# Optimization experiments

Hardware: AMD Instinct MI355X
Metric: run time of the kernel (lower is better)

The kernel has to match this reference:

```python
import jax, jax.numpy as jnp
import numpy as np

BANDS = np.array([0, 1, 2, 3, 4])
LOG_STDEVS = (0.0, 1.0)
CLAHE_MIN_STDEV = 1.0
K = 9      # CLAHE kernel size (hardcoded in module)
PAD = 4    # CLAHE reflect padding (hardcoded in module)


def _box_mean(x):
    # x: [B, C, H, W]; mean over KxK sliding window with reflect padding,
    # identical math to torch Unfold + mean over the K*K window axis.
    p = jnp.pad(x, ((0, 0), (0, 0), (PAD, PAD), (PAD, PAD)), mode='reflect')
    s = jax.lax.reduce_window(p, jnp.float32(0.0), jax.lax.add,
                              (1, 1, K, K), (1, 1, 1, 1), 'VALID')
    return s / (K * K)


def _clahe(img5d, min_stdev):
    # img5d: [B, C, 1, H, W]
    x = img5d[:, :, 0]
    res = x - _box_mean(x)
    stdev = jnp.sqrt(_box_mean(res * res))
    return (res / jnp.maximum(stdev, min_stdev))[:, :, None]


def setup_inputs() -> dict:
    key = jax.random.key(0)
    k1, k2 = jax.random.split(key, 2)
    B, C, H, W = 8, 5, 512, 512
    T = 3
    images = jax.random.normal(k1, (B, C, H, W), jnp.float32) * 10.0 + 100.0
    # background must be positive (asserted > 1e-6 in the module)
    background = jax.random.uniform(k2, (B, C, H, W), jnp.float32) * 50.0 + 50.0
    # learnable asinh params, initialized exactly as in __init__
    asinh_thresholds = jnp.tile(
        jnp.array([0.0, 1.0, 10.0], jnp.float32).reshape(1, 1, T, 1, 1),
        (1, C, 1, 1, 1))
    asinh_scales = jnp.full((1, C, T, 1, 1), np.log(0.1), jnp.float32)
    return {'images': images, 'background': background,
            'asinh_thresholds': asinh_thresholds, 'asinh_scales': asinh_scales}


def reference(images, background, asinh_thresholds, asinh_scales):
    raw = images[:, BANDS][:, :, None]        # [B, C, 1, H, W]
    bg = background[:, BANDS][:, :, None]     # [B, C, 1, H, W]
    inputs = [raw]                            # include_original=True; asinh on -> no raw background channel
    for t in LOG_STDEVS:
        off = (raw - bg) / jnp.sqrt(bg) - t
        inputs.append(jnp.log(jnp.maximum(off + 1.0, 1.0)))
    inputs.append(_clahe(raw, CLAHE_MIN_STDEV))
    inputs.append(jnp.arcsinh((raw - asinh_thresholds) * jnp.exp(asinh_scales)))
    return jnp.concatenate(inputs, axis=2)    # [B, C, 7, H, W]
```

## Files before the change

### kernel.cpp

```cpp
#include <hip/hip_runtime.h>
#include <math.h>

#define IMG_H 512
#define IMG_W 512
#define TS 32
#define NC 5
#define NB 8

__device__ __forceinline__ int reflect_idx(int i, int n) {
    if (i < 0) i = -i;
    if (i >= n) i = 2 * n - 2 - i;
    return i;
}

__device__ __forceinline__ float fast_log(float x) {
    return __builtin_amdgcn_logf(x) * 0.6931471805599453f;
}

__device__ __forceinline__ float fast_asinh(float v) {
    float a = fabsf(v);
    float r = fast_log(a + __builtin_amdgcn_sqrtf(fmaf(a, a, 1.0f)));
    return copysignf(r, v);
}

__global__ __launch_bounds__(256)
void imnorm_kernel(const float* __restrict__ img, const float* __restrict__ bgr,
                   const float* __restrict__ thr, const float* __restrict__ scl,
                   float* __restrict__ out)
{
    const int plane = blockIdx.z;
    const int c = plane % NC;
    const int h0 = blockIdx.y * TS;
    const int w0 = blockIdx.x * TS;
    const bool edge_w = (w0 == 0) || (w0 + TS == IMG_W);
    const bool edge_h = (h0 == 0) || (h0 + TS == IMG_H);

    const float* x  = img + (size_t)plane * IMG_H * IMG_W;
    const float* bg = bgr + (size_t)plane * IMG_H * IMG_W;
    float* op = out + (size_t)plane * 7 * IMG_H * IMG_W;

    const int t = threadIdx.y * 32 + threadIdx.x;

    __shared__ float xs[48][49];
    __shared__ float rs[40][41];
    __shared__ float pool[48 * 41];
    float (*h1)[41] = reinterpret_cast<float (*)[41]>(pool);
    float (*h2)[33] = reinterpret_cast<float (*)[33]>(pool);

    float s_thr[3], s_exp[3];
    #pragma unroll
    for (int j = 0; j < 3; ++j) {
        s_thr[j] = thr[c * 3 + j];
        s_exp[j] = __builtin_amdgcn_exp2f(scl[c * 3 + j] * 1.4426950408889634f);
    }

    if (!edge_w && !edge_h) {
        const float* src = x + (size_t)(h0 - 8) * IMG_W + (w0 - 8);
        #pragma unroll
        for (int k = 0; k < 9; ++k) {
            int i = t + k * 256;
            int r = i / 48, cc = i - r * 48;
            xs[r][cc] = src[r * IMG_W + cc];
        }
    } else {
        #pragma unroll
        for (int k = 0; k < 9; ++k) {
            int i = t + k * 256;
            int r = i / 48, cc = i - r * 48;
            int gr = reflect_idx(h0 - 8 + r, IMG_H);
            int gc = reflect_idx(w0 - 8 + cc, IMG_W);
            xs[r][cc] = x[gr * IMG_W + gc];
        }
    }
    __syncthreads();

    if (t < 240) {
        const int r  = t / 5;
        const int c0 = (t - r * 5) * 8;
        float s = xs[r][c0];
        #pragma unroll
        for (int d = 1; d < 9; ++d) s += xs[r][c0 + d];
        h1[r][c0] = s;
        #pragma unroll
        for (int k = 1; k < 8; ++k) {
            s += xs[r][c0 + 8 + k] - xs[r][c0 + k - 1];
            h1[r][c0 + k] = s;
        }
    }
    __syncthreads();

    if (t < 200) {
        const int seg = t / 40;
        const int cl  = t - seg * 40;
        const int r0  = seg * 8;
        float s = h1[r0][cl];
        #pragma unroll
        for (int d = 1; d < 9; ++d) s += h1[r0 + d][cl];
        rs[r0][cl] = xs[r0 + 4][cl + 4] - s * (1.0f / 81.0f);
        #pragma unroll
        for (int k = 1; k < 8; ++k) {
            s += h1[r0 + 8 + k][cl] - h1[r0 + k - 1][cl];
            rs[r0 + k][cl] = xs[r0 + k + 4][cl + 4] - s * (1.0f / 81.0f);
        }
    }
    __syncthreads();

    if (!edge_w) {
        #pragma unroll
        for (int k = 0; k < 5; ++k) {
            int i = t + k * 256;
            int rr = i >> 5, wl = i & 31;
            float s = 0.f;
            #pragma unroll
            for (int d = 0; d < 9; ++d) {
                float v = rs[rr][wl + d];
                s = fmaf(v, v, s);
            }
            h2[rr][wl] = s;
        }
    } else {
        #pragma unroll
        for (int k = 0; k < 5; ++k) {
            int i = t + k * 256;
            int rr = i >> 5, wl = i & 31;
            float s = 0.f;
            #pragma unroll
            for (int d = 0; d < 9; ++d) {
                int mc = reflect_idx(w0 + wl - 4 + d, IMG_W) - (w0 - 4);
                float v = rs[rr][mc];
                s = fmaf(v, v, s);
            }
            h2[rr][wl] = s;
        }
    }
    __syncthreads();

    const int wl  = threadIdx.x;
    const int hl0 = threadIdx.y * 4;

    float bgv[4];
    #pragma unroll
    for (int k = 0; k < 4; ++k)
        bgv[k] = bg[(size_t)(h0 + hl0 + k) * IMG_W + (w0 + wl)];

    float ssum[4];
    if (!edge_h) {
        float s = h2[hl0][wl];
        #pragma unroll
        for (int d = 1; d < 9; ++d) s += h2[hl0 + d][wl];
        ssum[0] = s;
        #pragma unroll
        for (int k = 1; k < 4; ++k) {
            s += h2[hl0 + 8 + k][wl] - h2[hl0 + k - 1][wl];
            ssum[k] = s;
        }
    } else {
        #pragma unroll
        for (int k = 0; k < 4; ++k) {
            const int h = h0 + hl0 + k;
            float s = 0.f;
            #pragma unroll
            for (int d = 0; d < 9; ++d) {
                int mr = reflect_idx(h - 4 + d, IMG_H) - (h0 - 4);
                s += h2[mr][wl];
            }
            ssum[k] = s;
        }
    }

    const size_t chs = (size_t)IMG_H * IMG_W;
    #pragma unroll
    for (int k = 0; k < 4; ++k) {
        const int hl = hl0 + k;
        const int h = h0 + hl, w = w0 + wl;

        float stdev = __builtin_amdgcn_sqrtf(fmaxf(ssum[k], 0.0f) * (1.0f / 81.0f));
        float resv  = rs[hl + 4][wl + 4];
        float clahe = resv * __builtin_amdgcn_rcpf(fmaxf(stdev, 1.0f));

        float raw  = xs[hl + 8][wl + 8];
        float off0 = (raw - bgv[k]) * __builtin_amdgcn_rsqf(bgv[k]);
        float l0 = fast_log(fmaxf(off0 + 1.0f, 1.0f));
        float l1 = fast_log(fmaxf(off0, 1.0f));

        const size_t base = (size_t)h * IMG_W + w;
        op[0 * chs + base] = raw;
        op[1 * chs + base] = l0;
        op[2 * chs + base] = l1;
        op[3 * chs + base] = clahe;
        #pragma unroll
        for (int j = 0; j < 3; ++j) {
            float v = (raw - s_thr[j]) * s_exp[j];
            op[(4 + j) * chs + base] = fast_asinh(v);
        }
    }
}

extern "C" void kernel_launch(void* const* d_in, const int* in_sizes, int n_in,
                              void* d_out, int out_size, void* d_ws, size_t ws_size,
                              hipStream_t stream) {
    const float* img = (const float*)d_in[0];
    const float* bg  = (const float*)d_in[1];
    const float* thr = (const float*)d_in[2];
    const float* scl = (const float*)d_in[3];
    float* out = (float*)d_out;

    dim3 grid(IMG_W / TS, IMG_H / TS, NB * NC);
    dim3 block(32, 8);
    hipLaunchKernelGGL(imnorm_kernel, grid, block, 0, stream,
                       img, bg, thr, scl, out);
}
```

Baseline: 354.8 us.

## Vectorize loads/stores with float4 and swap second box-sum pass order

Global loads of the interior tile, the background read and all seven output stores now use float4, with each thread owning four adjacent columns of one row instead of four rows of one column. The variance box filter now does its vertical pass first, as a running sum in shared memory, and the horizontal 9-tap sum is done in registers from float4 shared reads. Shared arrays get padded strides so the vector accesses stay 16-byte aligned. The aim is fewer memory instructions and wider transactions on a store-bound kernel, at the cost of possible shared-memory bank conflicts from the new strides and a changed edge-handling path.

```diff
diff --git a/kernel.cpp b/kernel.cpp
--- a/kernel.cpp
+++ b/kernel.cpp
@@ -41,11 +41,17 @@
 
     const int t = threadIdx.y * 32 + threadIdx.x;
 
-    __shared__ float xs[48][49];
-    __shared__ float rs[40][41];
+    __shared__ float xs[48][52];
+    __shared__ float rs[40][44];
     __shared__ float pool[48 * 41];
     float (*h1)[41] = reinterpret_cast<float (*)[41]>(pool);
-    float (*h2)[33] = reinterpret_cast<float (*)[33]>(pool);
+    float (*v2)[44] = reinterpret_cast<float (*)[44]>(pool);
+
+    const int r5  = t >> 3;
+    const int wl0 = (t & 7) * 4;
+
+    const float4 bgv = *reinterpret_cast<const float4*>(
+        bg + (size_t)(h0 + r5) * IMG_W + (w0 + wl0));
 
     float s_thr[3], s_exp[3];
     #pragma unroll
@@ -55,12 +61,15 @@
     }
 
     if (!edge_w && !edge_h) {
-        const float* src = x + (size_t)(h0 - 8) * IMG_W + (w0 - 8);
-        #pragma unroll
-        for (int k = 0; k < 9; ++k) {
+        const float4* src4 = reinterpret_cast<const float4*>(
+            x + (size_t)(h0 - 8) * IMG_W + (w0 - 8));
+        #pragma unroll
+        for (int k = 0; k < 3; ++k) {
             int i = t + k * 256;
-            int r = i / 48, cc = i - r * 48;
-            xs[r][cc] = src[r * IMG_W + cc];
+            if (i < 576) {
+                int r = i / 12, cc = i - r * 12;
+                *reinterpret_cast<float4*>(&xs[r][cc * 4]) = src4[r * 128 + cc];
+            }
         }
     } else {
         #pragma unroll
@@ -105,95 +114,97 @@
     }
     __syncthreads();
 
+    if (t < 160) {
+        const int seg = t / 40;
+        const int cl  = t - seg * 40;
+        const int r0  = seg * 8;
+        if (!edge_h) {
+            float v = rs[r0][cl];
+            float s = v * v;
+            #pragma unroll
+            for (int d = 1; d < 9; ++d) { v = rs[r0 + d][cl]; s = fmaf(v, v, s); }
+            v2[r0][cl] = s;
+            #pragma unroll
+            for (int k = 1; k < 8; ++k) {
+                float a = rs[r0 + 8 + k][cl];
+                float b = rs[r0 + k - 1][cl];
+                s = fmaf(a, a, fmaf(b, -b, s));
+                v2[r0 + k][cl] = s;
+            }
+        } else {
+            #pragma unroll
+            for (int k = 0; k < 8; ++k) {
+                const int hh = h0 + r0 + k;
+                float s = 0.f;
+                #pragma unroll
+                for (int d = 0; d < 9; ++d) {
+                    int mr = reflect_idx(hh - 4 + d, IMG_H) - (h0 - 4);
+                    float v = rs[mr][cl];
+                    s = fmaf(v, v, s);
+                }
+                v2[r0 + k][cl] = s;
+            }
+        }
+    }
+    __syncthreads();
+
+    float ssum[4];
     if (!edge_w) {
-        #pragma unroll
-        for (int k = 0; k < 5; ++k) {
-            int i = t + k * 256;
-            int rr = i >> 5, wl = i & 31;
+        const float* vr = &v2[r5][wl0];
+        float4 A  = *reinterpret_cast<const float4*>(vr);
+        float4 Bv = *reinterpret_cast<const float4*>(vr + 4);
+        float4 Cv = *reinterpret_cast<const float4*>(vr + 8);
+        float s0 = ((A.x + A.y) + (A.z + A.w)) + ((Bv.x + Bv.y) + (Bv.z + Bv.w)) + Cv.x;
+        ssum[0] = s0;
+        ssum[1] = s0      - A.x + Cv.y;
+        ssum[2] = ssum[1] - A.y + Cv.z;
+        ssum[3] = ssum[2] - A.z + Cv.w;
+    } else {
+        #pragma unroll
+        for (int j = 0; j < 4; ++j) {
+            const int w = w0 + wl0 + j;
             float s = 0.f;
             #pragma unroll
             for (int d = 0; d < 9; ++d) {
-                float v = rs[rr][wl + d];
-                s = fmaf(v, v, s);
-            }
-            h2[rr][wl] = s;
-        }
-    } else {
-        #pragma unroll
-        for (int k = 0; k < 5; ++k) {
-            int i = t + k * 256;
-            int rr = i >> 5, wl = i & 31;
-            float s = 0.f;
-            #pragma unroll
-            for (int d = 0; d < 9; ++d) {
-                int mc = reflect_idx(w0 + wl - 4 + d, IMG_W) - (w0 - 4);
-                float v = rs[rr][mc];
-                s = fmaf(v, v, s);
-            }
-            h2[rr][wl] = s;
-        }
-    }
-    __syncthreads();
-
-    const int wl  = threadIdx.x;
-    const int hl0 = threadIdx.y * 4;
-
-    float bgv[4];
+                int mc = reflect_idx(w - 4 + d, IMG_W) - (w0 - 4);
+                s += v2[r5][mc];
+            }
+            ssum[j] = s;
+        }
+    }
+
+    const float4 rsv = *reinterpret_cast<const float4*>(&rs[r5 + 4][wl0 + 4]);
+    const float4 xsv = *reinterpret_cast<const float4*>(&xs[r5 + 8][wl0 + 8]);
+
+    float o_raw[4], o_l0[4], o_l1[4], o_cl[4], o_a0[4], o_a1[4], o_a2[4];
+    const float rsa[4] = {rsv.x, rsv.y, rsv.z, rsv.w};
+    const float xsa[4] = {xsv.x, xsv.y, xsv.z, xsv.w};
+    const float bga[4] = {bgv.x, bgv.y, bgv.z, bgv.w};
+
     #pragma unroll
-    for (int k = 0; k < 4; ++k)
-        bgv[k] = bg[(size_t)(h0 + hl0 + k) * IMG_W + (w0 + wl)];
-
-    float ssum[4];
-    if (!edge_h) {
-        float s = h2[hl0][wl];
-        #pragma unroll
-        for (int d = 1; d < 9; ++d) s += h2[hl0 + d][wl];
-        ssum[0] = s;
-        #pragma unroll
-        for (int k = 1; k < 4; ++k) {
-            s += h2[hl0 + 8 + k][wl] - h2[hl0 + k - 1][wl];
-            ssum[k] = s;
-        }
-    } else {
-        #pragma unroll
-        for (int k = 0; k < 4; ++k) {
-            const int h = h0 + hl0 + k;
-            float s = 0.f;
-            #pragma unroll
-            for (int d = 0; d < 9; ++d) {
-                int mr = reflect_idx(h - 4 + d, IMG_H) - (h0 - 4);
-                s += h2[mr][wl];
-            }
-            ssum[k] = s;
-        }
+    for (int j = 0; j < 4; ++j) {
+        float stdev = __builtin_amdgcn_sqrtf(fmaxf(ssum[j], 0.0f) * (1.0f / 81.0f));
+        o_cl[j] = rsa[j] * __builtin_amdgcn_rcpf(fmaxf(stdev, 1.0f));
+
+        float raw = xsa[j];
+        o_raw[j] = raw;
+        float off0 = (raw - bga[j]) * __builtin_amdgcn_rsqf(bga[j]);
+        o_l0[j] = fast_log(fmaxf(off0 + 1.0f, 1.0f));
+        o_l1[j] = fast_log(fmaxf(off0, 1.0f));
+        o_a0[j] = fast_asinh((raw - s_thr[0]) * s_exp[0]);
+        o_a1[j] = fast_asinh((raw - s_thr[1]) * s_exp[1]);
+        o_a2[j] = fast_asinh((raw - s_thr[2]) * s_exp[2]);
     }
 
     const size_t chs = (size_t)IMG_H * IMG_W;
-    #pragma unroll
-    for (int k = 0; k < 4; ++k) {
-        const int hl = hl0 + k;
-        const int h = h0 + hl, w = w0 + wl;
-
-        float stdev = __builtin_amdgcn_sqrtf(fmaxf(ssum[k], 0.0f) * (1.0f / 81.0f));
-        float resv  = rs[hl + 4][wl + 4];
-        float clahe = resv * __builtin_amdgcn_rcpf(fmaxf(stdev, 1.0f));
-
-        float raw  = xs[hl + 8][wl + 8];
-        float off0 = (raw - bgv[k]) * __builtin_amdgcn_rsqf(bgv[k]);
-        float l0 = fast_log(fmaxf(off0 + 1.0f, 1.0f));
-        float l1 = fast_log(fmaxf(off0, 1.0f));
-
-        const size_t base = (size_t)h * IMG_W + w;
-        op[0 * chs + base] = raw;
-        op[1 * chs + base] = l0;
-        op[2 * chs + base] = l1;
-        op[3 * chs + base] = clahe;
-        #pragma unroll
-        for (int j = 0; j < 3; ++j) {
-            float v = (raw - s_thr[j]) * s_exp[j];
-            op[(4 + j) * chs + base] = fast_asinh(v);
-        }
-    }
+    float* p = op + (size_t)(h0 + r5) * IMG_W + (w0 + wl0);
+    *reinterpret_cast<float4*>(p) = make_float4(o_raw[0], o_raw[1], o_raw[2], o_raw[3]); p += chs;
+    *reinterpret_cast<float4*>(p) = make_float4(o_l0[0],  o_l0[1],  o_l0[2],  o_l0[3]);  p += chs;
+    *reinterpret_cast<float4*>(p) = make_float4(o_l1[0],  o_l1[1],  o_l1[2],  o_l1[3]);  p += chs;
+    *reinterpret_cast<float4*>(p) = make_float4(o_cl[0],  o_cl[1],  o_cl[2],  o_cl[3]);  p += chs;
+    *reinterpret_cast<float4*>(p) = make_float4(o_a0[0],  o_a0[1],  o_a0[2],  o_a0[3]);  p += chs;
+    *reinterpret_cast<float4*>(p) = make_float4(o_a1[0],  o_a1[1],  o_a1[2],  o_a1[3]);  p += chs;
+    *reinterpret_cast<float4*>(p) = make_float4(o_a2[0],  o_a2[1],  o_a2[2],  o_a2[3]);
 }
 
 extern "C" void kernel_launch(void* const* d_in, const int* in_sizes, int n_in,
```

New measurement: 359.0 us. About the same (+1.2%).
